# Kernel tuning notes

Measured on AMD Instinct MI355X. Metric: run time of the kernel, lower is better.

## Reference

```python
import jax, jax.numpy as jnp
import numpy as np
import math

NQ = 12          # num_qubits
DEPTH = 4        # circuit_depth
DIM = 2 ** NQ    # state_dim = 4096
B = 4096         # batch

# CNOT ladder: (i,i+1) plus wrap-around (n-1,0) when n>2 (as in _init_circuit_parameters)
CNOT_PAIRS = [(i, i + 1) for i in range(NQ - 1)] + ([(NQ - 1, 0)] if NQ > 2 else [])


def _rx(theta):
    c = jnp.cos(theta / 2).astype(jnp.complex64)
    s = jnp.sin(theta / 2).astype(jnp.complex64) * (-1j)
    return jnp.stack([jnp.stack([c, s]), jnp.stack([s, c])])


def _ry(phi):
    c = jnp.cos(phi / 2).astype(jnp.complex64)
    s = jnp.sin(phi / 2).astype(jnp.complex64)
    return jnp.stack([jnp.stack([c, -s]), jnp.stack([s, c])])


def _rz(lam):
    lamc = lam.astype(jnp.complex64)
    e0 = jnp.exp(-1j * lamc / 2)
    e1 = jnp.exp(1j * lamc / 2)
    z = jnp.zeros((), jnp.complex64)
    return jnp.stack([jnp.stack([e0, z]), jnp.stack([z, e1])])


def _apply_1q(state, gate, q):
    # state: [B] + [2]*NQ, qubit q lives on axis q+1 (kron order: qubit 0 most significant)
    ax = q + 1
    s = jnp.moveaxis(state, ax, -1)
    s = jnp.einsum('ab,...b->...a', gate, s)
    return jnp.moveaxis(s, -1, ax)


def _apply_cnot(state, control, target):
    # flip target bit on the control=1 half of the state vector
    ac, at = control + 1, target + 1
    s0 = jnp.take(state, jnp.array([0]), axis=ac)
    s1 = jnp.take(state, jnp.array([1]), axis=ac)
    s1 = jnp.flip(s1, axis=at)
    return jnp.concatenate([s0, s1], axis=ac)


def setup_inputs() -> dict:
    key = jax.random.key(0)
    k1, k2, k3, k4 = jax.random.split(key, 4)
    return {
        'input_data': jax.random.normal(k1, (B, DIM), dtype=jnp.float32),
        'angles_x': jax.random.normal(k2, (DEPTH, NQ), dtype=jnp.float32) * 0.5,
        'angles_y': jax.random.normal(k3, (DEPTH, NQ), dtype=jnp.float32) * 0.5,
        'angles_z': jax.random.normal(k4, (DEPTH, NQ), dtype=jnp.float32) * 0.5,
    }


def reference(input_data, angles_x, angles_y, angles_z):
    # --- amplitude encoding (faithful to quantum_weight_memory) ---
    w = jnp.abs(input_data[:, :DIM])                      # [B, D]
    D = w.shape[1]
    s = jnp.sum(w, axis=1, keepdims=True)
    wn = jnp.where(s > 1e-8, w / jnp.sqrt(jnp.maximum(s, 1e-8)),
                   jnp.full_like(w, 1.0 / math.sqrt(D)))
    state = jnp.zeros((w.shape[0], DIM), jnp.complex64).at[:, 0].set(1.0)
    state = state.at[:, :D].set(wn.astype(jnp.complex64))
    norm = jnp.sqrt(jnp.sum(jnp.abs(state) ** 2, axis=1, keepdims=True))
    state = jnp.where(norm > 1e-8, state / jnp.maximum(norm, 1e-8), state)

    # --- parametrized circuit, applied as local state-vector updates ---
    state = state.reshape((state.shape[0],) + (2,) * NQ)
    for layer in range(DEPTH):
        for q in range(NQ):
            state = _apply_1q(state, _rx(angles_x[layer, q]), q)
            state = _apply_1q(state, _ry(angles_y[layer, q]), q)
            state = _apply_1q(state, _rz(angles_z[layer, q]), q)
        for c, t in CNOT_PAIRS:
            state = _apply_cnot(state, c, t)
    state = state.reshape(-1, DIM)

    # --- measurement ---
    probs = jnp.abs(state) ** 2
    return jnp.sqrt(probs[:, :DIM])
```

## Files before the change

kernel.cpp:

```cpp
#include <hip/hip_runtime.h>
#include <math.h>

#define DIM 4096

typedef _Float16 v8h __attribute__((ext_vector_type(8)));
typedef float v4f __attribute__((ext_vector_type(4)));
typedef unsigned int v2u __attribute__((ext_vector_type(2)));

__device__ __forceinline__ unsigned pkrtz(float a, float b) {
  return __builtin_bit_cast(unsigned, __builtin_amdgcn_cvt_pkrtz(a, b));
}

__device__ __forceinline__ int adr(int row, int off) {
  return ((row << 6) | off) ^ ((((row >> 1) ^ (row >> 5)) & 3) << 4)
                            ^ (((row >> 4) & 1) << 6);
}


template <int PASS, bool FOLD, bool LAST>
__device__ __forceinline__ void do_pass(const char* __restrict__ src, char* __restrict__ dst,
                                        const v8h* __restrict__ Af, int mat, int t) {
  const int lane = t & 63, wv = t >> 6;
  const int m = lane & 15, q = lane >> 4;
  const int qb = q & 1, pm = q >> 1;
  const v8h b_re = Af[(mat * 2 + 0) * 64 + lane];
  const v8h b_im = Af[(mat * 2 + 1) * 64 + lane];
  const int gm = (m ^ (m >> 1)) & 15;
  const bool qh = (q & 1) != 0;
#pragma unroll
  for (int tt = 0; tt < 4; ++tt) {
    const int t4 = wv * 4 + tt;
    v8h a;
    if constexpr (PASS == 0 && FOLD) {
      const int t4g = t4 ^ (t4 >> 1);
      const int gq2 = ((q ^ (q >> 1)) & 3) ^ ((tt & 1) ? 3 : 0);
      const int r0 = ((t4g ^ ((m & 1) << 3)) << 4) | gm;
      const uint4 E = *(const uint4*)(src + adr(r0, gq2 * 16));
      const uint4 O = *(const uint4*)(src + adr(r0 ^ 8, gq2 * 16));
      uint4 av;
      av.x = qh ? E.z : E.x;
      av.y = qh ? O.w : O.y;
      av.z = qh ? E.y : E.w;
      av.w = qh ? O.x : O.z;
      a = __builtin_bit_cast(v8h, av);
    } else if constexpr (PASS == 0) {
      a = *(const v8h*)(src + adr(t4 * 16 + m, q * 16));
    } else {
      const uint4 r = *(const uint4*)(src + adr(t4 * 16 + m, (2 * qb + pm) * 16));
      const v2u s0 = __builtin_amdgcn_permlane32_swap(r.x, r.z, false, false);
      const v2u s1 = __builtin_amdgcn_permlane32_swap(r.y, r.w, false, false);
      uint4 av;
      av.x = s0.x; av.y = s1.x; av.z = s0.y; av.w = s1.y;
      a = __builtin_bit_cast(v8h, av);
    }
    const v4f cre = __builtin_amdgcn_mfma_f32_16x16x32_f16(a, b_re, (v4f){0.f, 0.f, 0.f, 0.f}, 0, 0, 0);
    const v4f cim = __builtin_amdgcn_mfma_f32_16x16x32_f16(a, b_im, (v4f){0.f, 0.f, 0.f, 0.f}, 0, 0, 0);
    const int wrow = m * 16 + t4;
    if constexpr (PASS < 2) {
      uint4 w;
      w.x = pkrtz(cre[0], cre[1]);
      w.y = pkrtz(cre[2], cre[3]);
      w.z = pkrtz(cim[0], cim[1]);
      w.w = pkrtz(cim[2], cim[3]);
      *(uint4*)(dst + adr(wrow, q * 16)) = w;
    } else if constexpr (!LAST) {
      uint4 w;
      w.x = pkrtz(cre[0], cim[0]);
      w.y = pkrtz(cre[1], cim[1]);
      w.z = pkrtz(cre[2], cim[2]);
      w.w = pkrtz(cre[3], cim[3]);
      *(uint4*)(dst + adr(wrow, q * 16)) = w;
    } else {
      uint2 wr, wi;
      wr.x = pkrtz(cre[0], cre[1]);
      wr.y = pkrtz(cre[2], cre[3]);
      wi.x = pkrtz(cim[0], cim[1]);
      wi.y = pkrtz(cim[2], cim[3]);
      *(uint2*)(dst + adr(wrow, q * 8)) = wr;
      *(uint2*)(dst + adr(wrow, 32 + q * 8)) = wi;
    }
  }
}

__global__ void make_gates2(const float* __restrict__ ax, const float* __restrict__ ay,
                            const float* __restrict__ az, _Float16* __restrict__ Aw) {
  __shared__ float g4[48][4];
  const int id = threadIdx.x;
  if (id < 48) {
    float th = 0.5f * ax[id], ph = 0.5f * ay[id], lm = 0.5f * az[id];
    float c = cosf(th), s = sinf(th);
    float cy = cosf(ph), sy = sinf(ph);
    float cl = cosf(lm), sl = sinf(lm);
    float m00r = cy * c, m00i = sy * s;
    float m01r = -sy * c, m01i = -cy * s;
    g4[id][0] = cl * m00r + sl * m00i;
    g4[id][1] = cl * m00i - sl * m00r;
    g4[id][2] = cl * m01r + sl * m01i;
    g4[id][3] = cl * m01i - sl * m01r;
  }
  __syncthreads();
  const int mat = id >> 6, lane = id & 63;
  const int m = lane & 15, q = lane >> 4;
  const int layer = mat / 3, pass = mat % 3, qbase = pass * 4;
#pragma unroll
  for (int j = 0; j < 8; ++j) {
    int p, ty;
    if (pass == 0) { p = q * 4 + (j >> 1); ty = j & 1; }
    else { p = (q * 8 + j) & 15; ty = (q >= 2) ? 1 : 0; }
    float cr = 1.f, ci = 0.f;
#pragma unroll
    for (int bp = 3; bp >= 0; --bp) {
      const int qq = qbase + (3 - bp);
      const int ib = (m >> bp) & 1, kb = (p >> bp) & 1;
      const float* gg = g4[layer * 12 + qq];
      float er, ei;
      if (ib == 0 && kb == 0) { er = gg[0]; ei = gg[1]; }
      else if (ib == 0 && kb == 1) { er = gg[2]; ei = gg[3]; }
      else if (ib == 1 && kb == 0) { er = -gg[2]; ei = gg[3]; }
      else { er = gg[0]; ei = -gg[1]; }
      const float nr = cr * er - ci * ei, ni = cr * ei + ci * er;
      cr = nr; ci = ni;
    }
    const float reval = ty ? -ci : cr;
    const float imval = ty ? cr : ci;
    Aw[((mat * 2 + 0) * 64 + lane) * 8 + j] = (_Float16)reval;
    Aw[((mat * 2 + 1) * 64 + lane) * 8 + j] = (_Float16)imval;
  }
}

__global__ __launch_bounds__(256, 4) void qsim5(const float* __restrict__ x,
                                                const v8h* __restrict__ Af,
                                                float* __restrict__ out) {
  __shared__ __align__(16) char buf[2][16384];
  const int t = threadIdx.x;
  const int b = blockIdx.x;
  const float* xb = x + (size_t)b * DIM;

  float wa[16];
  float sw = 0.f, sw2 = 0.f;
#pragma unroll
  for (int j = 0; j < 16; ++j) {
    float aa = fabsf(xb[t + (j << 8)]);
    wa[j] = aa; sw += aa; sw2 += aa * aa;
  }
#pragma unroll
  for (int off = 32; off; off >>= 1) {
    sw += __shfl_down(sw, off, 64);
    sw2 += __shfl_down(sw2, off, 64);
  }
  float* red = (float*)buf[1];
  if ((t & 63) == 0) { red[t >> 6] = sw; red[4 + (t >> 6)] = sw2; }
  __syncthreads();
  sw = (red[0] + red[1]) + (red[2] + red[3]);
  sw2 = (red[4] + red[5]) + (red[6] + red[7]);

  float sc = 0.f;
  const bool ok = (sw > 1e-8f);
  if (ok) {
    float wnscale = rsqrtf(fmaxf(sw, 1e-8f));
    float norm = sqrtf(sw2 / sw);
    sc = ((norm > 1e-8f) ? (wnscale / fmaxf(norm, 1e-8f)) : wnscale) * 64.0f;
  }
  const float off0 = ok ? 0.f : 1.f;
  {
    const int row = ((t & 15) << 4) | (t >> 4);
#pragma unroll
    for (int Q = 0; Q < 4; ++Q) {
      uint4 w;
      w.x = pkrtz(fmaf(wa[Q * 4 + 0], sc, off0), 0.f);
      w.y = pkrtz(fmaf(wa[Q * 4 + 1], sc, off0), 0.f);
      w.z = pkrtz(fmaf(wa[Q * 4 + 2], sc, off0), 0.f);
      w.w = pkrtz(fmaf(wa[Q * 4 + 3], sc, off0), 0.f);
      *(uint4*)(buf[0] + adr(row, Q * 16)) = w;
    }
  }
  __syncthreads();

  char* s = buf[0];
  char* d = buf[1];
  do_pass<0, false, false>(s, d, Af, 0, t); __syncthreads();
  do_pass<1, false, false>(d, s, Af, 1, t); __syncthreads();
  do_pass<2, false, false>(s, d, Af, 2, t); __syncthreads();
  { char* tmp = s; s = d; d = tmp; }
#pragma unroll 1
  for (int l = 1; l < 3; ++l) {
    do_pass<0, true, false>(s, d, Af, l * 3 + 0, t); __syncthreads();
    do_pass<1, false, false>(d, s, Af, l * 3 + 1, t); __syncthreads();
    do_pass<2, false, false>(s, d, Af, l * 3 + 2, t); __syncthreads();
    char* tmp = s; s = d; d = tmp;
  }
  do_pass<0, true, false>(s, d, Af, 9, t); __syncthreads();
  do_pass<1, false, false>(d, s, Af, 10, t); __syncthreads();
  do_pass<2, false, true>(s, d, Af, 11, t); __syncthreads();
  { char* tmp = s; s = d; d = tmp; }

  typedef _Float16 v4h __attribute__((ext_vector_type(4)));
  float* ob = out + (size_t)b * DIM;
  {
    const int g = t ^ (t >> 1);
    const int re_row = (g & 15) * 16 + ((g >> 4) & 15);
    const int ro = re_row ^ 8;
    const int offA = (t & 1) ? 24 : 0;
    const int offB = (t & 1) ? 16 : 8;
    const v4h E0 = *(const v4h*)(s + adr(re_row, offA));
    const v4h E1 = *(const v4h*)(s + adr(re_row, offB));
    const v4h E2 = *(const v4h*)(s + adr(re_row, offA ^ 24));
    const v4h E3 = *(const v4h*)(s + adr(re_row, offB ^ 24));
    const v4h O0 = *(const v4h*)(s + adr(ro, offA));
    const v4h O1 = *(const v4h*)(s + adr(ro, offB));
    const v4h O2 = *(const v4h*)(s + adr(ro, offA ^ 24));
    const v4h O3 = *(const v4h*)(s + adr(ro, offB ^ 24));
    const v4h IE0 = *(const v4h*)(s + adr(re_row, 32 + offA));
    const v4h IE1 = *(const v4h*)(s + adr(re_row, 32 + offB));
    const v4h IE2 = *(const v4h*)(s + adr(re_row, 32 + (offA ^ 24)));
    const v4h IE3 = *(const v4h*)(s + adr(re_row, 32 + (offB ^ 24)));
    const v4h IO0 = *(const v4h*)(s + adr(ro, 32 + offA));
    const v4h IO1 = *(const v4h*)(s + adr(ro, 32 + offB));
    const v4h IO2 = *(const v4h*)(s + adr(ro, 32 + (offA ^ 24)));
    const v4h IO3 = *(const v4h*)(s + adr(ro, 32 + (offB ^ 24)));
#define MAG(J, VR, VI, IDX)                                                       \
  {                                                                               \
    const float re_ = (float)VR[IDX], im_ = (float)VI[IDX];                       \
    ob[((J) << 8) | t] = __builtin_amdgcn_sqrtf(re_ * re_ + im_ * im_) * 0.015625f; \
  }
    MAG(0, E0, IE0, 0)  MAG(2, E0, IE0, 3)  MAG(4, E1, IE1, 2)  MAG(6, E1, IE1, 1)
    MAG(8, E2, IE2, 0)  MAG(10, E2, IE2, 3) MAG(12, E3, IE3, 2) MAG(14, E3, IE3, 1)
    MAG(1, O0, IO0, 1)  MAG(3, O0, IO0, 2)  MAG(5, O1, IO1, 3)  MAG(7, O1, IO1, 0)
    MAG(9, O2, IO2, 1)  MAG(11, O2, IO2, 2) MAG(13, O3, IO3, 3) MAG(15, O3, IO3, 0)
#undef MAG
  }
}

extern "C" void kernel_launch(void* const* d_in, const int* in_sizes, int n_in,
                              void* d_out, int out_size, void* d_ws, size_t ws_size,
                              hipStream_t stream) {
  const float* x = (const float*)d_in[0];
  const float* ax = (const float*)d_in[1];
  const float* ay = (const float*)d_in[2];
  const float* az = (const float*)d_in[3];
  _Float16* Aw = (_Float16*)d_ws;
  make_gates2<<<1, 768, 0, stream>>>(ax, ay, az, Aw);
  qsim5<<<4096, 256, 0, stream>>>(x, (const v8h*)Aw, (float*)d_out);
}
```

Baseline: 154.9 us.

## Fuse first two MFMA passes per layer using in-register lane permutes

Merges passes 0 and 1 of each circuit layer into a single routine. The pass-0 MFMA output is packed and redistributed across lanes with permlane32/permlane16 swaps so it can feed the pass-1 MFMA directly, removing one shared-memory round trip and one barrier per layer. Results for four tiles are buffered in registers and written in a transposed layout, which raises register pressure and changes the LDS write pattern. Correctness depends on the permute mapping matching the layout the old intermediate store and reload produced.

```diff
diff --git a/kernel.cpp b/kernel.cpp
--- a/kernel.cpp
+++ b/kernel.cpp
@@ -17,21 +17,23 @@
 }
 
 
-template <int PASS, bool FOLD, bool LAST>
-__device__ __forceinline__ void do_pass(const char* __restrict__ src, char* __restrict__ dst,
-                                        const v8h* __restrict__ Af, int mat, int t) {
+template <bool FOLD>
+__device__ __forceinline__ void pass01(const char* __restrict__ src, char* __restrict__ dst,
+                                       const v8h* __restrict__ Af, int mat, int t) {
   const int lane = t & 63, wv = t >> 6;
   const int m = lane & 15, q = lane >> 4;
-  const int qb = q & 1, pm = q >> 1;
-  const v8h b_re = Af[(mat * 2 + 0) * 64 + lane];
-  const v8h b_im = Af[(mat * 2 + 1) * 64 + lane];
+  const bool qh = (q & 1) != 0;
+  const v8h b0_re = Af[((mat) * 2 + 0) * 64 + lane];
+  const v8h b0_im = Af[((mat) * 2 + 1) * 64 + lane];
+  const v8h b1_re = Af[((mat + 1) * 2 + 0) * 64 + lane];
+  const v8h b1_im = Af[((mat + 1) * 2 + 1) * 64 + lane];
   const int gm = (m ^ (m >> 1)) & 15;
-  const bool qh = (q & 1) != 0;
+  v4f ar[4], ai[4];
 #pragma unroll
   for (int tt = 0; tt < 4; ++tt) {
     const int t4 = wv * 4 + tt;
-    v8h a;
-    if constexpr (PASS == 0 && FOLD) {
+    v8h a0;
+    if constexpr (FOLD) {
       const int t4g = t4 ^ (t4 >> 1);
       const int gq2 = ((q ^ (q >> 1)) & 3) ^ ((tt & 1) ? 3 : 0);
       const int r0 = ((t4g ^ ((m & 1) << 3)) << 4) | gm;
@@ -42,28 +44,59 @@
       av.y = qh ? O.w : O.y;
       av.z = qh ? E.y : E.w;
       av.w = qh ? O.x : O.z;
-      a = __builtin_bit_cast(v8h, av);
-    } else if constexpr (PASS == 0) {
-      a = *(const v8h*)(src + adr(t4 * 16 + m, q * 16));
+      a0 = __builtin_bit_cast(v8h, av);
     } else {
-      const uint4 r = *(const uint4*)(src + adr(t4 * 16 + m, (2 * qb + pm) * 16));
-      const v2u s0 = __builtin_amdgcn_permlane32_swap(r.x, r.z, false, false);
-      const v2u s1 = __builtin_amdgcn_permlane32_swap(r.y, r.w, false, false);
-      uint4 av;
-      av.x = s0.x; av.y = s1.x; av.z = s0.y; av.w = s1.y;
-      a = __builtin_bit_cast(v8h, av);
-    }
+      a0 = *(const v8h*)(src + adr(t4 * 16 + m, q * 16));
+    }
+    const v4f cre = __builtin_amdgcn_mfma_f32_16x16x32_f16(a0, b0_re, (v4f){0.f, 0.f, 0.f, 0.f}, 0, 0, 0);
+    const v4f cim = __builtin_amdgcn_mfma_f32_16x16x32_f16(a0, b0_im, (v4f){0.f, 0.f, 0.f, 0.f}, 0, 0, 0);
+    const unsigned R0 = pkrtz(cre[0], cre[1]);
+    const unsigned R1 = pkrtz(cre[2], cre[3]);
+    const unsigned I0 = pkrtz(cim[0], cim[1]);
+    const unsigned I1 = pkrtz(cim[2], cim[3]);
+    const v2u PQ0 = __builtin_amdgcn_permlane32_swap(R0, I0, false, false);
+    const v2u PQ1 = __builtin_amdgcn_permlane32_swap(R1, I1, false, false);
+    const v2u W02 = __builtin_amdgcn_permlane16_swap(PQ0.x, PQ0.y, false, false);
+    const v2u W13 = __builtin_amdgcn_permlane16_swap(PQ1.x, PQ1.y, false, false);
+    uint4 a1u;
+    a1u.x = W02.x; a1u.y = W13.x; a1u.z = W02.y; a1u.w = W13.y;
+    const v8h a1 = __builtin_bit_cast(v8h, a1u);
+    ar[tt] = __builtin_amdgcn_mfma_f32_16x16x32_f16(a1, b1_re, (v4f){0.f, 0.f, 0.f, 0.f}, 0, 0, 0);
+    ai[tt] = __builtin_amdgcn_mfma_f32_16x16x32_f16(a1, b1_im, (v4f){0.f, 0.f, 0.f, 0.f}, 0, 0, 0);
+  }
+  const int colbase = m * 16 + q * 4;
+#pragma unroll
+  for (int r2 = 0; r2 < 4; ++r2) {
+    uint4 w;
+    w.x = pkrtz(ar[0][r2], ar[1][r2]);
+    w.y = pkrtz(ar[2][r2], ar[3][r2]);
+    w.z = pkrtz(ai[0][r2], ai[1][r2]);
+    w.w = pkrtz(ai[2][r2], ai[3][r2]);
+    *(uint4*)(dst + adr(colbase + r2, wv * 16)) = w;
+  }
+}
+
+template <bool LAST>
+__device__ __forceinline__ void pass2f(const char* __restrict__ src, char* __restrict__ dst,
+                                       const v8h* __restrict__ Af, int mat, int t) {
+  const int lane = t & 63, wv = t >> 6;
+  const int m = lane & 15, q = lane >> 4;
+  const int qb = q & 1, pm = q >> 1;
+  const v8h b_re = Af[(mat * 2 + 0) * 64 + lane];
+  const v8h b_im = Af[(mat * 2 + 1) * 64 + lane];
+#pragma unroll
+  for (int tt = 0; tt < 4; ++tt) {
+    const int t4 = wv * 4 + tt;
+    const uint4 r = *(const uint4*)(src + adr(t4 * 16 + m, (2 * qb + pm) * 16));
+    const v2u s0 = __builtin_amdgcn_permlane32_swap(r.x, r.z, false, false);
+    const v2u s1 = __builtin_amdgcn_permlane32_swap(r.y, r.w, false, false);
+    uint4 av;
+    av.x = s0.x; av.y = s1.x; av.z = s0.y; av.w = s1.y;
+    const v8h a = __builtin_bit_cast(v8h, av);
     const v4f cre = __builtin_amdgcn_mfma_f32_16x16x32_f16(a, b_re, (v4f){0.f, 0.f, 0.f, 0.f}, 0, 0, 0);
     const v4f cim = __builtin_amdgcn_mfma_f32_16x16x32_f16(a, b_im, (v4f){0.f, 0.f, 0.f, 0.f}, 0, 0, 0);
     const int wrow = m * 16 + t4;
-    if constexpr (PASS < 2) {
-      uint4 w;
-      w.x = pkrtz(cre[0], cre[1]);
-      w.y = pkrtz(cre[2], cre[3]);
-      w.z = pkrtz(cim[0], cim[1]);
-      w.w = pkrtz(cim[2], cim[3]);
-      *(uint4*)(dst + adr(wrow, q * 16)) = w;
-    } else if constexpr (!LAST) {
+    if constexpr (!LAST) {
       uint4 w;
       w.x = pkrtz(cre[0], cim[0]);
       w.y = pkrtz(cre[1], cim[1]);
@@ -128,7 +161,7 @@
   }
 }
 
-__global__ __launch_bounds__(256, 4) void qsim5(const float* __restrict__ x,
+__global__ __launch_bounds__(256, 4) void qsim6(const float* __restrict__ x,
                                                 const v8h* __restrict__ Af,
                                                 float* __restrict__ out) {
   __shared__ __align__(16) char buf[2][16384];
@@ -178,21 +211,15 @@
 
   char* s = buf[0];
   char* d = buf[1];
-  do_pass<0, false, false>(s, d, Af, 0, t); __syncthreads();
-  do_pass<1, false, false>(d, s, Af, 1, t); __syncthreads();
-  do_pass<2, false, false>(s, d, Af, 2, t); __syncthreads();
-  { char* tmp = s; s = d; d = tmp; }
+  pass01<false>(s, d, Af, 0, t); __syncthreads();
+  pass2f<false>(d, s, Af, 2, t); __syncthreads();
 #pragma unroll 1
   for (int l = 1; l < 3; ++l) {
-    do_pass<0, true, false>(s, d, Af, l * 3 + 0, t); __syncthreads();
-    do_pass<1, false, false>(d, s, Af, l * 3 + 1, t); __syncthreads();
-    do_pass<2, false, false>(s, d, Af, l * 3 + 2, t); __syncthreads();
-    char* tmp = s; s = d; d = tmp;
-  }
-  do_pass<0, true, false>(s, d, Af, 9, t); __syncthreads();
-  do_pass<1, false, false>(d, s, Af, 10, t); __syncthreads();
-  do_pass<2, false, true>(s, d, Af, 11, t); __syncthreads();
-  { char* tmp = s; s = d; d = tmp; }
+    pass01<true>(s, d, Af, l * 3, t); __syncthreads();
+    pass2f<false>(d, s, Af, l * 3 + 2, t); __syncthreads();
+  }
+  pass01<true>(s, d, Af, 9, t); __syncthreads();
+  pass2f<true>(d, s, Af, 11, t); __syncthreads();
 
   typedef _Float16 v4h __attribute__((ext_vector_type(4)));
   float* ob = out + (size_t)b * DIM;
@@ -240,5 +267,5 @@
   const float* az = (const float*)d_in[3];
   _Float16* Aw = (_Float16*)d_ws;
   make_gates2<<<1, 768, 0, stream>>>(ax, ay, az, Aw);
-  qsim5<<<4096, 256, 0, stream>>>(x, (const v8h*)Aw, (float*)d_out);
-}
+  qsim6<<<4096, 256, 0, stream>>>(x, (const v8h*)Aw, (float*)d_out);
+}
```

Result: faster. 149.1 us (-3.8%).
